# Kernel optimization log

Hardware: AMD Instinct MI355X
Metric: run time of the kernel (lower is better)

Reference implementation:

```python
import jax, jax.numpy as jnp
import numpy as np

VOCAB = 50257
EMB = 256
HID = 512
NCLS = 50257


def setup_inputs() -> dict:
    key = jax.random.key(0)
    ks = jax.random.split(key, 6)
    x = jax.random.randint(ks[0], (64, 512), 0, VOCAB, dtype=jnp.int32)
    emb_weight = jax.random.normal(ks[1], (VOCAB, EMB), dtype=jnp.float32) * 0.01
    # torch Linear: weight [out_features, in_features], bias [out_features]
    lim_w = 1.0 / np.sqrt(EMB + HID)
    W_weight = jax.random.uniform(ks[2], (4 * HID, EMB + HID), jnp.float32, -lim_w, lim_w)
    W_bias = jax.random.uniform(ks[3], (4 * HID,), jnp.float32, -lim_w, lim_w)
    lim_fc = 1.0 / np.sqrt(HID)
    fc_weight = jax.random.uniform(ks[4], (NCLS, HID), jnp.float32, -lim_fc, lim_fc)
    fc_bias = jax.random.uniform(ks[5], (NCLS,), jnp.float32, -lim_fc, lim_fc)
    return {"x": x, "emb_weight": emb_weight, "W_weight": W_weight,
            "W_bias": W_bias, "fc_weight": fc_weight, "fc_bias": fc_bias}


def reference(x, emb_weight, W_weight, W_bias, fc_weight, fc_bias):
    B, S = x.shape
    H = W_weight.shape[0] // 4
    embedded = emb_weight[x]                     # [B, S, E]
    Wx = W_weight[:, :EMB]                       # [4H, E]
    Wh = W_weight[:, EMB:]                       # [4H, H]

    def step(carry, x_t):
        h, C = carry
        gates = x_t @ Wx.T + h @ Wh.T + W_bias   # [B, 4H]
        f, i, o, c_tilde = jnp.split(gates, 4, axis=1)
        f = jax.nn.sigmoid(f)
        i = jax.nn.sigmoid(i)
        o = jax.nn.sigmoid(o)
        c_tilde = jnp.tanh(c_tilde)
        C_new = f * C + i * c_tilde
        h_new = o * jnp.tanh(C_new)
        return (h_new, C_new), None

    h0 = jnp.zeros((B, H), embedded.dtype)
    C0 = jnp.zeros((B, H), embedded.dtype)
    (h, _), _ = jax.lax.scan(step, (h0, C0), jnp.swapaxes(embedded, 0, 1))
    return h @ fc_weight.T + fc_bias             # [B, num_classes]
```

## Files before the change

### kernel.cpp

```cpp
#include <hip/hip_runtime.h>
#include <stdint.h>

#define EMBD   256
#define HID    512
#define KTOT   768
#define NCLS   50257
#define STEPS  512

#define NGROUP 8
#define GB     8
#define BPG    32
#define HS     16
#define UPITCH 776
#define RP     129

typedef float f32x4  __attribute__((ext_vector_type(4)));
typedef short bf16x8 __attribute__((ext_vector_type(8)));
typedef unsigned long long u64;

__device__ __forceinline__ unsigned bf16_rne(float f) {
  unsigned u = __float_as_uint(f);
  return (u + 0x7FFFu + ((u >> 16) & 1u)) >> 16;
}
__device__ __forceinline__ float bf16_to_f32(unsigned b) {
  return __uint_as_float(b << 16);
}

__global__ void emb_prep(const int* __restrict__ x, const float* __restrict__ emb,
                         unsigned* __restrict__ emb_hl) {
  int base = blockIdx.x * 4;
  int k = threadIdx.x;
  for (int it = 0; it < 4; ++it) {
    int tok = base + it;
    int id = x[tok];
    float w = emb[(size_t)id * EMBD + k];
    unsigned hb = bf16_rne(w);
    unsigned lb = bf16_rne(w - bf16_to_f32(hb));
    emb_hl[(size_t)tok * EMBD + k] = hb | (lb << 16);
  }
}

__global__ __launch_bounds__(512, 2) void lstm_persist(
    const float* __restrict__ Ww, const float* __restrict__ Wb,
    const unsigned* __restrict__ emb_hl,
    u64* __restrict__ hbuf,
    unsigned short* __restrict__ h_hi, unsigned short* __restrict__ h_lo)
{
  __shared__ __align__(16) unsigned short u_hi[16 * UPITCH];
  __shared__ __align__(16) unsigned short u_lo[16 * UPITCH];
  __shared__ __align__(16) float red[32 * RP];

  const int tid  = threadIdx.x;
  const int wave = tid >> 6;
  const int lane = tid & 63;
  const int g = blockIdx.x & 7;
  const int s = blockIdx.x >> 3;

  for (int i = tid; i < 16 * UPITCH; i += 512) { u_hi[i] = 0; u_lo[i] = 0; }

  const int cn = lane & 15;
  const int qk = (lane >> 4) * 8;
  bf16x8 whi[3][4], wlo[3][4];
#pragma unroll
  for (int i = 0; i < 3; ++i) {
    int kt = wave + i * 8;
    int k0 = kt * 32 + qk;
#pragma unroll
    for (int nt = 0; nt < 4; ++nt) {
      int row = nt * 512 + s * HS + cn;
      const float* src = Ww + (size_t)row * KTOT + k0;
      float4 w0 = *(const float4*)src;
      float4 w1 = *(const float4*)(src + 4);
      float wv[8] = {w0.x, w0.y, w0.z, w0.w, w1.x, w1.y, w1.z, w1.w};
#pragma unroll
      for (int j = 0; j < 8; ++j) {
        unsigned hb = bf16_rne(wv[j]);
        unsigned lb = bf16_rne(wv[j] - bf16_to_f32(hb));
        whi[i][nt][j] = (short)hb;
        wlo[i][nt][j] = (short)lb;
      }
    }
  }

  const float bias = Wb[(lane >> 4) * 512 + s * HS + (lane & 15)];

  float Cst = 0.0f;

  const unsigned* embg = emb_hl + (size_t)(g * GB) * STEPS * EMBD;
  u64* hg = hbuf + (size_t)g * 2 * GB * HID;

  __syncthreads();

  for (int step = 0; step < STEPS; ++step) {
    {
      int f0 = tid * 4;
      int b = f0 >> 8, k0 = f0 & 255;
      uint4 v = *(const uint4*)(embg + ((size_t)b * STEPS + step) * EMBD + k0);
      unsigned h01 = (v.x & 0xFFFFu) | ((v.y & 0xFFFFu) << 16);
      unsigned h23 = (v.z & 0xFFFFu) | ((v.w & 0xFFFFu) << 16);
      unsigned l01 = (v.x >> 16) | (v.y & 0xFFFF0000u);
      unsigned l23 = (v.z >> 16) | (v.w & 0xFFFF0000u);
      *(uint2*)&u_hi[b * UPITCH + k0] = make_uint2(h01, h23);
      *(uint2*)&u_lo[b * UPITCH + k0] = make_uint2(l01, l23);
    }
    __syncthreads();

    f32x4 acc[4] = {{0.f,0.f,0.f,0.f},{0.f,0.f,0.f,0.f},
                    {0.f,0.f,0.f,0.f},{0.f,0.f,0.f,0.f}};

    {
      int k0 = wave * 32 + qk;
      int m = lane & 15;
      bf16x8 ahi = *(const bf16x8*)&u_hi[m * UPITCH + k0];
      bf16x8 alo = *(const bf16x8*)&u_lo[m * UPITCH + k0];
#pragma unroll
      for (int nt = 0; nt < 4; ++nt) {
        acc[nt] = __builtin_amdgcn_mfma_f32_16x16x32_bf16(ahi, whi[0][nt], acc[nt], 0, 0, 0);
        acc[nt] = __builtin_amdgcn_mfma_f32_16x16x32_bf16(ahi, wlo[0][nt], acc[nt], 0, 0, 0);
        acc[nt] = __builtin_amdgcn_mfma_f32_16x16x32_bf16(alo, whi[0][nt], acc[nt], 0, 0, 0);
      }
    }

    {
      const u64* hp = hg + ((size_t)(step & 1) * GB + wave) * HID;
      u64 v[8];
      const unsigned want = (unsigned)step;
      while (true) {
        bool ok = true;
#pragma unroll
        for (int j = 0; j < 8; ++j)
          v[j] = __hip_atomic_load(&hp[j * 64 + lane], __ATOMIC_RELAXED,
                                   __HIP_MEMORY_SCOPE_AGENT);
#pragma unroll
        for (int j = 0; j < 8; ++j)
          ok &= ((unsigned)(v[j] >> 32) == want);
        if (ok) break;
        __builtin_amdgcn_s_sleep(1);
      }
#pragma unroll
      for (int j = 0; j < 8; ++j) {
        unsigned w32 = (unsigned)v[j];
        u_hi[wave * UPITCH + EMBD + j * 64 + lane] = (unsigned short)(w32 & 0xFFFFu);
        u_lo[wave * UPITCH + EMBD + j * 64 + lane] = (unsigned short)(w32 >> 16);
      }
    }
    __syncthreads();

#pragma unroll
    for (int i = 1; i < 3; ++i) {
      int k0 = (wave + i * 8) * 32 + qk;
      int m = lane & 15;
      bf16x8 ahi = *(const bf16x8*)&u_hi[m * UPITCH + k0];
      bf16x8 alo = *(const bf16x8*)&u_lo[m * UPITCH + k0];
#pragma unroll
      for (int nt = 0; nt < 4; ++nt) {
        acc[nt] = __builtin_amdgcn_mfma_f32_16x16x32_bf16(ahi, whi[i][nt], acc[nt], 0, 0, 0);
        acc[nt] = __builtin_amdgcn_mfma_f32_16x16x32_bf16(ahi, wlo[i][nt], acc[nt], 0, 0, 0);
        acc[nt] = __builtin_amdgcn_mfma_f32_16x16x32_bf16(alo, whi[i][nt], acc[nt], 0, 0, 0);
      }
    }
    if (lane < 32) {
#pragma unroll
      for (int nt = 0; nt < 4; ++nt)
        *(f32x4*)&red[(wave * 4 + nt) * RP + lane * 4] = acc[nt];
    }
    __syncthreads();

    float gsum = bias;
    {
      int tq = lane >> 4;
      int rbase = ((((wave >> 2) << 4) | (lane & 15)) << 2) + (wave & 3);
#pragma unroll
      for (int w = 0; w < 8; ++w)
        gsum += red[(w * 4 + tq) * RP + rbase];
    }

    float scl = (lane >= 48) ? 2.0f : 1.0f;
    float y = 1.0f / (1.0f + __expf(-gsum * scl));
    float act = (lane >= 48) ? (2.0f * y - 1.0f) : y;
    float ig = __shfl(act, lane + 16);
    float og = __shfl(act, lane + 32);
    float cg = __shfl(act, lane + 48);
    if (lane < 16) {
      Cst = act * Cst + ig * cg;
      float t2 = 1.0f / (1.0f + __expf(-2.0f * Cst));
      float hv = og * (2.0f * t2 - 1.0f);
      unsigned hb = bf16_rne(hv);
      unsigned lb = bf16_rne(hv - bf16_to_f32(hb));
      u64 pack = ((u64)(unsigned)(step + 1) << 32) | (u64)(hb | (lb << 16));
      __hip_atomic_store(
          &hg[((size_t)((step + 1) & 1) * GB + wave) * HID + s * HS + lane],
          pack, __ATOMIC_RELAXED, __HIP_MEMORY_SCOPE_AGENT);
      if (step == STEPS - 1) {
        int m = g * GB + wave, k = s * HS + lane;
        h_hi[m * HID + k] = (unsigned short)hb;
        h_lo[m * HID + k] = (unsigned short)lb;
      }
    }
  }
}

__device__ __forceinline__ void cvt8(const float4& a, const float4& b,
                                     bf16x8& hi, bf16x8& lo) {
  float v[8] = {a.x, a.y, a.z, a.w, b.x, b.y, b.z, b.w};
#pragma unroll
  for (int j = 0; j < 8; ++j) {
    unsigned hb = bf16_rne(v[j]);
    hi[j] = (short)hb;
    lo[j] = (short)bf16_rne(v[j] - bf16_to_f32(hb));
  }
}

__global__ __launch_bounds__(512) void fc_mfma(
    const unsigned short* __restrict__ h_hi, const unsigned short* __restrict__ h_lo,
    const float* __restrict__ fcw, const float* __restrict__ fcb,
    float* __restrict__ out)
{
  const int tid = threadIdx.x, wave = tid >> 6, lane = tid & 63;
  const int cn = lane & 15;
  const int qk = (lane >> 4) * 8;
  const int cls  = blockIdx.x * 128 + wave * 16 + cn;
  const int clsc = cls < NCLS ? cls : NCLS - 1;

  f32x4 acc[4] = {{0.f,0.f,0.f,0.f},{0.f,0.f,0.f,0.f},
                  {0.f,0.f,0.f,0.f},{0.f,0.f,0.f,0.f}};
#pragma unroll 2
  for (int kt = 0; kt < 16; ++kt) {
    int k0 = kt * 32 + qk;
    const float* bp = fcw + (size_t)clsc * HID + k0;
    float4 b0 = *(const float4*)bp;
    float4 b1 = *(const float4*)(bp + 4);
    bf16x8 bhi, blo;
    cvt8(b0, b1, bhi, blo);
#pragma unroll
    for (int mt = 0; mt < 4; ++mt) {
      bf16x8 ahi = *(const bf16x8*)&h_hi[(size_t)(mt * 16 + cn) * HID + k0];
      bf16x8 alo = *(const bf16x8*)&h_lo[(size_t)(mt * 16 + cn) * HID + k0];
      acc[mt] = __builtin_amdgcn_mfma_f32_16x16x32_bf16(ahi, bhi, acc[mt], 0, 0, 0);
      acc[mt] = __builtin_amdgcn_mfma_f32_16x16x32_bf16(ahi, blo, acc[mt], 0, 0, 0);
      acc[mt] = __builtin_amdgcn_mfma_f32_16x16x32_bf16(alo, bhi, acc[mt], 0, 0, 0);
    }
  }
  if (cls < NCLS) {
    float bias = fcb[cls];
#pragma unroll
    for (int mt = 0; mt < 4; ++mt)
#pragma unroll
      for (int j = 0; j < 4; ++j) {
        int m = mt * 16 + (lane >> 4) * 4 + j;
        out[(size_t)m * NCLS + cls] = acc[mt][j] + bias;
      }
  }
}

extern "C" void kernel_launch(void* const* d_in, const int* in_sizes, int n_in,
                              void* d_out, int out_size, void* d_ws, size_t ws_size,
                              hipStream_t stream) {
  const int*   x   = (const int*)d_in[0];
  const float* emb = (const float*)d_in[1];
  const float* Ww  = (const float*)d_in[2];
  const float* Wb  = (const float*)d_in[3];
  const float* fcw = (const float*)d_in[4];
  const float* fcb = (const float*)d_in[5];
  float* out = (float*)d_out;

  char* ws = (char*)d_ws;
  u64*            hbuf   = (u64*)ws;
  unsigned short* h_hi   = (unsigned short*)(ws + 524288);
  unsigned short* h_lo   = (unsigned short*)(ws + 524288 + 65536);
  unsigned*       emb_hl = (unsigned*)(ws + 524288 + 131072);

  hipMemsetAsync(hbuf, 0, 524288, stream);

  emb_prep<<<8192, 256, 0, stream>>>(x, emb, emb_hl);

  void* args[] = { (void*)&Ww, (void*)&Wb, (void*)&emb_hl,
                   (void*)&hbuf, (void*)&h_hi, (void*)&h_lo };
  hipLaunchCooperativeKernel((void*)lstm_persist, dim3(256), dim3(512),
                             args, 0, stream);

  fc_mfma<<<(NCLS + 127) / 128, 512, 0, stream>>>(h_hi, h_lo, fcw, fcb, out);
}
```

Baseline: 1.386 ms.

## Pack hi/lo activations into one MFMA tile and drop a block barrier

The batch has only 8 rows, so the hi and lo bf16 halves of the activations are now stacked into a single 16-row tile. Each k-slice needs two MFMAs (against the hi and lo weights) instead of three. The two row halves are then summed with a cross-lane shuffle. The hidden-state layout in shared memory is remapped so each wave reads only the columns it wrote, which removes one __syncthreads per step. The reduction buffer is double-buffered to avoid a write-after-read hazard across steps. In exchange, the hi*lo product term is now computed too, and the shuffle adds ALU work to every step.

```diff
diff --git a/kernel.cpp b/kernel.cpp
--- a/kernel.cpp
+++ b/kernel.cpp
@@ -46,9 +46,8 @@
     u64* __restrict__ hbuf,
     unsigned short* __restrict__ h_hi, unsigned short* __restrict__ h_lo)
 {
-  __shared__ __align__(16) unsigned short u_hi[16 * UPITCH];
-  __shared__ __align__(16) unsigned short u_lo[16 * UPITCH];
-  __shared__ __align__(16) float red[32 * RP];
+  __shared__ __align__(16) unsigned short u[16 * UPITCH];
+  __shared__ __align__(16) float red[2][32 * RP];
 
   const int tid  = threadIdx.x;
   const int wave = tid >> 6;
@@ -56,7 +55,7 @@
   const int g = blockIdx.x & 7;
   const int s = blockIdx.x >> 3;
 
-  for (int i = tid; i < 16 * UPITCH; i += 512) { u_hi[i] = 0; u_lo[i] = 0; }
+  for (int i = tid; i < 16 * UPITCH; i += 512) u[i] = 0;
 
   const int cn = lane & 15;
   const int qk = (lane >> 4) * 8;
@@ -88,6 +87,10 @@
 
   const unsigned* embg = emb_hl + (size_t)(g * GB) * STEPS * EMBD;
   u64* hg = hbuf + (size_t)g * 2 * GB * HID;
+
+  const int phalf = lane >> 5;
+  const int pcol  = lane & 31;
+  const int ubase = phalf * 256 + wave * 32 + pcol;
 
   __syncthreads();
 
@@ -100,8 +103,8 @@
       unsigned h23 = (v.z & 0xFFFFu) | ((v.w & 0xFFFFu) << 16);
       unsigned l01 = (v.x >> 16) | (v.y & 0xFFFF0000u);
       unsigned l23 = (v.z >> 16) | (v.w & 0xFFFF0000u);
-      *(uint2*)&u_hi[b * UPITCH + k0] = make_uint2(h01, h23);
-      *(uint2*)&u_lo[b * UPITCH + k0] = make_uint2(l01, l23);
+      *(uint2*)&u[b * UPITCH + k0]       = make_uint2(h01, h23);
+      *(uint2*)&u[(b + 8) * UPITCH + k0] = make_uint2(l01, l23);
     }
     __syncthreads();
 
@@ -111,58 +114,61 @@
     {
       int k0 = wave * 32 + qk;
       int m = lane & 15;
-      bf16x8 ahi = *(const bf16x8*)&u_hi[m * UPITCH + k0];
-      bf16x8 alo = *(const bf16x8*)&u_lo[m * UPITCH + k0];
+      bf16x8 a = *(const bf16x8*)&u[m * UPITCH + k0];
 #pragma unroll
       for (int nt = 0; nt < 4; ++nt) {
-        acc[nt] = __builtin_amdgcn_mfma_f32_16x16x32_bf16(ahi, whi[0][nt], acc[nt], 0, 0, 0);
-        acc[nt] = __builtin_amdgcn_mfma_f32_16x16x32_bf16(ahi, wlo[0][nt], acc[nt], 0, 0, 0);
-        acc[nt] = __builtin_amdgcn_mfma_f32_16x16x32_bf16(alo, whi[0][nt], acc[nt], 0, 0, 0);
-      }
-    }
-
-    {
-      const u64* hp = hg + ((size_t)(step & 1) * GB + wave) * HID;
+        acc[nt] = __builtin_amdgcn_mfma_f32_16x16x32_bf16(a, whi[0][nt], acc[nt], 0, 0, 0);
+        acc[nt] = __builtin_amdgcn_mfma_f32_16x16x32_bf16(a, wlo[0][nt], acc[nt], 0, 0, 0);
+      }
+    }
+
+    {
+      const u64* hp = hg + (size_t)(step & 1) * GB * HID;
       u64 v[8];
       const unsigned want = (unsigned)step;
       while (true) {
         bool ok = true;
 #pragma unroll
-        for (int j = 0; j < 8; ++j)
-          v[j] = __hip_atomic_load(&hp[j * 64 + lane], __ATOMIC_RELAXED,
+        for (int b = 0; b < 8; ++b)
+          v[b] = __hip_atomic_load(&hp[b * HID + ubase], __ATOMIC_RELAXED,
                                    __HIP_MEMORY_SCOPE_AGENT);
 #pragma unroll
-        for (int j = 0; j < 8; ++j)
-          ok &= ((unsigned)(v[j] >> 32) == want);
+        for (int b = 0; b < 8; ++b)
+          ok &= ((unsigned)(v[b] >> 32) == want);
         if (ok) break;
         __builtin_amdgcn_s_sleep(1);
       }
 #pragma unroll
-      for (int j = 0; j < 8; ++j) {
-        unsigned w32 = (unsigned)v[j];
-        u_hi[wave * UPITCH + EMBD + j * 64 + lane] = (unsigned short)(w32 & 0xFFFFu);
-        u_lo[wave * UPITCH + EMBD + j * 64 + lane] = (unsigned short)(w32 >> 16);
-      }
-    }
-    __syncthreads();
+      for (int b = 0; b < 8; ++b) {
+        unsigned w32 = (unsigned)v[b];
+        u[b * UPITCH + EMBD + ubase]       = (unsigned short)(w32 & 0xFFFFu);
+        u[(b + 8) * UPITCH + EMBD + ubase] = (unsigned short)(w32 >> 16);
+      }
+    }
 
 #pragma unroll
     for (int i = 1; i < 3; ++i) {
       int k0 = (wave + i * 8) * 32 + qk;
       int m = lane & 15;
-      bf16x8 ahi = *(const bf16x8*)&u_hi[m * UPITCH + k0];
-      bf16x8 alo = *(const bf16x8*)&u_lo[m * UPITCH + k0];
+      bf16x8 a = *(const bf16x8*)&u[m * UPITCH + k0];
 #pragma unroll
       for (int nt = 0; nt < 4; ++nt) {
-        acc[nt] = __builtin_amdgcn_mfma_f32_16x16x32_bf16(ahi, whi[i][nt], acc[nt], 0, 0, 0);
-        acc[nt] = __builtin_amdgcn_mfma_f32_16x16x32_bf16(ahi, wlo[i][nt], acc[nt], 0, 0, 0);
-        acc[nt] = __builtin_amdgcn_mfma_f32_16x16x32_bf16(alo, whi[i][nt], acc[nt], 0, 0, 0);
-      }
-    }
+        acc[nt] = __builtin_amdgcn_mfma_f32_16x16x32_bf16(a, whi[i][nt], acc[nt], 0, 0, 0);
+        acc[nt] = __builtin_amdgcn_mfma_f32_16x16x32_bf16(a, wlo[i][nt], acc[nt], 0, 0, 0);
+      }
+    }
+
+#pragma unroll
+    for (int nt = 0; nt < 4; ++nt)
+#pragma unroll
+      for (int r = 0; r < 4; ++r)
+        acc[nt][r] += __shfl(acc[nt][r], lane + 32);
+
+    float* redp = &red[step & 1][0];
     if (lane < 32) {
 #pragma unroll
       for (int nt = 0; nt < 4; ++nt)
-        *(f32x4*)&red[(wave * 4 + nt) * RP + lane * 4] = acc[nt];
+        *(f32x4*)&redp[(wave * 4 + nt) * RP + lane * 4] = acc[nt];
     }
     __syncthreads();
 
@@ -172,7 +178,7 @@
       int rbase = ((((wave >> 2) << 4) | (lane & 15)) << 2) + (wave & 3);
 #pragma unroll
       for (int w = 0; w < 8; ++w)
-        gsum += red[(w * 4 + tq) * RP + rbase];
+        gsum += redp[(w * 4 + tq) * RP + rbase];
     }
 
     float scl = (lane >= 48) ? 2.0f : 1.0f;
```

New measurement: 1.504 ms. +8.5%, slower.
